# Performance work log

Hardware: AMD Instinct MI355X
Metric: run time of the kernel (lower is better)

The kernel has to match this reference:

```python
import jax, jax.numpy as jnp
import numpy as np

B, L, C, N, DEPTH, OUT = 32, 4096, 128, 64, 4, 1
EPS = 1e-5


def setup_inputs() -> dict:
    key = jax.random.key(0)
    ks = jax.random.split(key, 8)
    x = jax.random.normal(ks[0], (B, L, C), dtype=jnp.float32)
    # S4D parameters, stacked over depth
    # dt log-uniform in [1e-3, 1e-1]
    u = jax.random.uniform(ks[1], (DEPTH, C), dtype=jnp.float32)
    log_dt = u * (np.log(1e-1) - np.log(1e-3)) + np.log(1e-3)
    A_real = jnp.log(0.5 * jnp.ones((DEPTH, C, N), dtype=jnp.float32))  # A = -exp(A_real)+i*A_imag
    A_imag = jnp.broadcast_to(np.pi * jnp.arange(N, dtype=jnp.float32), (DEPTH, C, N)).copy()
    C_re = jax.random.normal(ks[2], (DEPTH, C, N), dtype=jnp.float32) * 0.5
    C_im = jax.random.normal(ks[3], (DEPTH, C, N), dtype=jnp.float32) * 0.5
    Dskip = jax.random.normal(ks[4], (DEPTH, C), dtype=jnp.float32)
    norm_w = jnp.ones((DEPTH, C), dtype=jnp.float32)
    norm_b = jnp.zeros((DEPTH, C), dtype=jnp.float32)
    head_w = jax.random.normal(ks[5], (C, OUT), dtype=jnp.float32) / np.sqrt(C)
    head_b = jnp.zeros((OUT,), dtype=jnp.float32)
    return {"x": x, "log_dt": log_dt, "A_real": A_real, "A_imag": A_imag,
            "C_re": C_re, "C_im": C_im, "Dskip": Dskip,
            "norm_w": norm_w, "norm_b": norm_b, "head_w": head_w, "head_b": head_b}


def _s4d(x, log_dt, A_real, A_imag, C_re, C_im, Dskip):
    # x: [B, L, C]; per-channel diagonal SSM (S4D, ZOH discretization)
    Lx = x.shape[1]
    dt = jnp.exp(log_dt)                               # [C]
    A = -jnp.exp(A_real) + 1j * A_imag                 # [C, N]
    dtA = A * dt[:, None]                              # [C, N]
    Cbar = (C_re + 1j * C_im) * (jnp.exp(dtA) - 1.0) / A  # [C, N] = C * B_bar
    t = jnp.arange(Lx, dtype=jnp.float32)
    # Vandermonde kernel: K[c, l] = 2*Re sum_n Cbar[c,n] * exp(dtA[c,n]*l)
    K = 2.0 * jnp.real(jnp.einsum('cn,cnl->cl', Cbar, jnp.exp(dtA[:, :, None] * t)))  # [C, L]
    # FFT long convolution (causal, linear conv via zero-pad to 2L)
    nfft = 2 * Lx
    xf = jnp.fft.rfft(x, n=nfft, axis=1)               # [B, F, C]
    Kf = jnp.fft.rfft(K, n=nfft, axis=-1)              # [C, F]
    y = jnp.fft.irfft(xf * Kf.T[None], n=nfft, axis=1)[:, :Lx, :]
    return y + x * Dskip                               # D skip connection


def _layernorm(x, w, b):
    mu = jnp.mean(x, axis=-1, keepdims=True)
    var = jnp.mean(jnp.square(x - mu), axis=-1, keepdims=True)
    return (x - mu) * jax.lax.rsqrt(var + EPS) * w + b


def reference(x, log_dt, A_real, A_imag, C_re, C_im, Dskip, norm_w, norm_b, head_w, head_b):
    for d in range(DEPTH):
        residual = x
        y = _s4d(x, log_dt[d], A_real[d], A_imag[d], C_re[d], C_im[d], Dskip[d])
        x = _layernorm(y + residual, norm_w[d], norm_b[d])
    return x @ head_w + head_b                          # [B, L, OUT]
```

## Files before the change

kernel.cpp:

```cpp
#include <hip/hip_runtime.h>
#include <hip/hip_bf16.h>


#define BB     32
#define LL     4096
#define CC     128
#define NN     64
#define DEPTH_ 4
#define EPSV   1e-5f

typedef __attribute__((ext_vector_type(8))) short short8;
typedef __attribute__((ext_vector_type(4))) short short4v;
typedef __attribute__((ext_vector_type(4))) float f32x4;
typedef __hip_bfloat16 bf16;

#define MFMA(a, b, c) __builtin_amdgcn_mfma_f32_16x16x32_bf16(a, b, c, 0, 0, 0)

__device__ __forceinline__ bf16 tobf(float x) { return __float2bfloat16(x); }
__device__ __forceinline__ short bfbits(float x) {
    union { bf16 b; short s; } u; u.b = __float2bfloat16(x); return u.s;
}

__global__ __launch_bounds__(64) void p0_kernel(
    const float* __restrict__ log_dt, const float* __restrict__ A_real,
    const float* __restrict__ A_imag, const float* __restrict__ C_re,
    const float* __restrict__ C_im, float2* __restrict__ lam,
    float2* __restrict__ dta, float2* __restrict__ cb2,
    float2* __restrict__ lamT)
{
    int d = blockIdx.y, c = blockIdx.x, n = threadIdx.x;
    int idx = (d * CC + c) * NN + n;
    float dt  = expf(log_dt[d * CC + c]);
    float Ar  = -expf(A_real[idx]);
    float Ai  = A_imag[idx];
    float dtr = dt * Ar, dti = dt * Ai;
    float e   = expf(dtr);
    float lr  = e * cosf(dti), li = e * sinf(dti);
    float m    = Ar * Ar + Ai * Ai;
    float inv  = 1.0f / m;
    float numr = lr - 1.0f, numi = li;
    float br   = (numr * Ar + numi * Ai) * inv;
    float bi   = (numi * Ar - numr * Ai) * inv;
    float cre  = C_re[idx], cim = C_im[idx];
    lam[idx]  = make_float2(lr, li);
    dta[idx]  = make_float2(dtr, dti);
    cb2[idx]  = make_float2(2.0f * (cre * br - cim * bi),
                            2.0f * (cre * bi + cim * br));
    float eT = expf(64.0f * dtr);
    lamT[idx] = make_float2(eT * cosf(64.0f * dti), eT * sinf(64.0f * dti));
}

__global__ __launch_bounds__(64) void p1_kernel(
    const float2* __restrict__ cb2, const float2* __restrict__ lam,
    float* __restrict__ Kloc)
{
    __shared__ float st[64 * 65];
    int d = blockIdx.y, c = blockIdx.x, n = threadIdx.x;
    float2 p = cb2[(d * CC + c) * NN + n];
    float2 l = lam[(d * CC + c) * NN + n];
    for (int t = 0; t < 64; ++t) {
        st[t * 65 + n] = p.x;
        float nr = p.x * l.x - p.y * l.y;
        p.y = p.x * l.y + p.y * l.x;
        p.x = nr;
    }
    __syncthreads();
    float s = 0.0f;
#pragma unroll 16
    for (int j = 0; j < 64; ++j) s += st[n * 65 + j];
    Kloc[(d * CC + c) * 64 + n] = s;
}

__global__ __launch_bounds__(256) void p2v_kernel(
    const float2* __restrict__ dta, bf16* __restrict__ Vp)
{
    int t = blockIdx.x * 256 + threadIdx.x;
    int e = t & 7, l = (t >> 3) & 63, ks = (t >> 9) & 1;
    int nf = (t >> 10) & 7, c = (t >> 13) & 127, d = t >> 20;
    int q = nf * 16 + (l & 15);
    int k = ks * 32 + (l >> 4) * 8 + e;
    int n = q >> 1;
    float2 a = dta[(d * CC + c) * NN + n];
    float p  = (float)(63 - k);
    float mag = expf(p * a.x);
    float ang = p * a.y;
    float val = (q & 1) ? mag * sinf(ang) : mag * cosf(ang);
    Vp[t] = tobf(val);
}

__global__ __launch_bounds__(256) void p2w_kernel(
    const float2* __restrict__ dta, const float2* __restrict__ cb2,
    const float* __restrict__ Kloc, const float* __restrict__ Dskip,
    bf16* __restrict__ W2p)
{
    int t = blockIdx.x * 256 + threadIdx.x;
    int e = t & 7, l = (t >> 3) & 63;
    int r = t >> 9;
    int ks = r % 6; r /= 6;
    int nf = r & 3; r >>= 2;
    int c  = r & 127;
    int d  = r >> 7;
    int i = nf * 16 + (l & 15);
    int k = ks * 32 + (l >> 4) * 8 + e;
    float val;
    if (k < 64) {
        val = (k <= i) ? Kloc[(d * CC + c) * 64 + (i - k)] : 0.0f;
        if (k == i) val += Dskip[d * CC + c] + 1.0f;
    } else {
        int q = k - 64, n = q >> 1;
        float2 a  = dta[(d * CC + c) * NN + n];
        float2 cb = cb2[(d * CC + c) * NN + n];
        float p   = (float)(i + 1);
        float mag = expf(p * a.x);
        float ang = p * a.y;
        float re = mag * cosf(ang), im = mag * sinf(ang);
        float wre = cb.x * re - cb.y * im;
        float wim = cb.x * im + cb.y * re;
        val = (q & 1) ? -wim : wre;
    }
    W2p[t] = tobf(val);
}

__global__ __launch_bounds__(256) void transpose_kernel(
    const float* __restrict__ x, bf16* __restrict__ xt)
{
    __shared__ float t[64][65];
    int ct = blockIdx.x, lt = blockIdx.y, b = blockIdx.z;
    int tx = threadIdx.x & 63, ty = threadIdx.x >> 6;
    const size_t xbase = ((size_t)b * LL + (size_t)lt * 64) * CC + (size_t)ct * 64;
#pragma unroll
    for (int i = 0; i < 16; ++i)
        t[ty + 4 * i][tx] = x[xbase + (size_t)(ty + 4 * i) * CC + tx];
    __syncthreads();
    const size_t obase = ((size_t)b * CC + (size_t)ct * 64) * LL + (size_t)lt * 64;
#pragma unroll
    for (int i = 0; i < 16; ++i)
        xt[obase + (size_t)(ty + 4 * i) * LL + tx] = tobf(t[tx][ty + 4 * i]);
}

__global__ __launch_bounds__(512) void ks_kernel(
    const bf16* __restrict__ u, bf16* __restrict__ v,
    const bf16* __restrict__ Vp, const bf16* __restrict__ W2p,
    const float2* __restrict__ lamT)
{
    const int c  = blockIdx.x;
    const int w  = threadIdx.x >> 6;
    const int l  = threadIdx.x & 63;
    const int b  = blockIdx.y * 8 + w;
    const int bc = b * CC + c;
    const bf16* xrow = u + (size_t)bc * LL;
    bf16*       vrow = v + (size_t)bc * LL;

    __shared__ short Wl[8192 + 12288];
    __shared__ short Sp[8][16 * 136];

    {
        uint4*       dst  = (uint4*)Wl;
        const uint4* srcV = (const uint4*)(Vp  + (size_t)c * 8192);
        const uint4* srcW = (const uint4*)(W2p + (size_t)c * 12288);
        int tid = threadIdx.x;
#pragma unroll
        for (int i = 0; i < 2; ++i)
            dst[tid + 512 * i] = srcV[tid + 512 * i];
#pragma unroll
        for (int i = 0; i < 3; ++i)
            dst[1024 + tid + 512 * i] = srcW[tid + 512 * i];
    }
    __syncthreads();

    short* S = Sp[w];
    const short* W2l = Wl + 8192;
    const int mloc = l & 15;
    const int koff = (l >> 4) * 8;
    float2 lt = lamT[c * NN + l];
    float sr = 0.f, si = 0.f;

#pragma unroll 1
    for (int g = 0; g < 4; ++g) {
        const bf16* xg = xrow + (g * 16 + mloc) * 64;

        {
            short8 xf0 = *(const short8*)(xg + koff);
            short8 xf1 = *(const short8*)(xg + 32 + koff);
#pragma unroll
            for (int h = 0; h < 2; ++h) {
                f32x4 acc[4];
#pragma unroll
                for (int j = 0; j < 4; ++j) acc[j] = (f32x4){0.f, 0.f, 0.f, 0.f};
#pragma unroll
                for (int j = 0; j < 4; ++j) {
                    int nf = h * 4 + j;
                    short8 vf0 = *(const short8*)(&Wl[((nf * 2 + 0) * 64 + l) * 8]);
                    short8 vf1 = *(const short8*)(&Wl[((nf * 2 + 1) * 64 + l) * 8]);
                    acc[j] = MFMA(vf0, xf0, acc[j]);
                    acc[j] = MFMA(vf1, xf1, acc[j]);
                }
#pragma unroll
                for (int j = 0; j < 4; ++j) {
                    int nf = h * 4 + j;
                    short4v t;
                    t[0] = bfbits(acc[j][0]); t[1] = bfbits(acc[j][1]);
                    t[2] = bfbits(acc[j][2]); t[3] = bfbits(acc[j][3]);
                    *(short4v*)(&S[mloc * 136 + nf * 16 + (l >> 4) * 4]) = t;
                }
            }
        }
        asm volatile("" ::: "memory");

#pragma unroll
        for (int k = 0; k < 16; ++k) {
            uint pk = *(const uint*)(&S[k * 136 + 2 * l]);
            union { short2 s2; uint uu; } o;
            o.s2.x = bfbits(sr); o.s2.y = bfbits(si);
            *(uint*)(&S[k * 136 + 2 * l]) = o.uu;
            float pr = __uint_as_float(pk << 16);
            float pi = __uint_as_float(pk & 0xffff0000u);
            float nr = fmaf(lt.x, sr, fmaf(-lt.y, si, pr));
            si = fmaf(lt.x, si, fmaf(lt.y, sr, pi));
            sr = nr;
        }
        asm volatile("" ::: "memory");

        f32x4 o[4];
#pragma unroll
        for (int nf = 0; nf < 4; ++nf) o[nf] = (f32x4){0.f, 0.f, 0.f, 0.f};
#pragma unroll
        for (int ks = 0; ks < 6; ++ks) {
            short8 xf;
            if (ks < 2)
                xf = *(const short8*)(xg + ks * 32 + koff);
            else
                xf = *(const short8*)(&S[mloc * 136 + (ks - 2) * 32 + koff]);
#pragma unroll
            for (int nf = 0; nf < 4; ++nf) {
                short8 wf = *(const short8*)(&W2l[((nf * 6 + ks) * 64 + l) * 8]);
                o[nf] = MFMA(wf, xf, o[nf]);
            }
        }
#pragma unroll
        for (int nf = 0; nf < 4; ++nf) {
            short4v t;
            t[0] = bfbits(o[nf][0]); t[1] = bfbits(o[nf][1]);
            t[2] = bfbits(o[nf][2]); t[3] = bfbits(o[nf][3]);
            *(short4v*)(vrow + (g * 16 + mloc) * 64 + nf * 16 + (l >> 4) * 4) = t;
        }
    }
}

__global__ __launch_bounds__(256) void ln_kernel(
    const bf16* __restrict__ v, bf16* __restrict__ outx,
    const float* __restrict__ w, const float* __restrict__ bta,
    const float* __restrict__ headw, const float* __restrict__ headb,
    float* __restrict__ fout, int isfinal)
{
    __shared__ float tile[CC][65];
    __shared__ float r1[4][64];
    __shared__ float r2[4][64];
    __shared__ float mrs[2][64];
    int b    = blockIdx.y;
    int l0   = blockIdx.x * 64;
    int lane = threadIdx.x & 63;
    int cg   = threadIdx.x >> 6;
    float sum = 0.0f, sq = 0.0f;
#pragma unroll
    for (int ci = 0; ci < 32; ++ci) {
        int c = cg * 32 + ci;
        float val = __bfloat162float(v[((size_t)b * CC + c) * LL + l0 + lane]);
        tile[c][lane] = val;
        sum += val;
        sq = fmaf(val, val, sq);
    }
    r1[cg][lane] = sum;
    r2[cg][lane] = sq;
    __syncthreads();
    if (cg == 0) {
        float s = r1[0][lane] + r1[1][lane] + r1[2][lane] + r1[3][lane];
        float q = r2[0][lane] + r2[1][lane] + r2[2][lane] + r2[3][lane];
        float mean = s * (1.0f / CC);
        float var  = q * (1.0f / CC) - mean * mean;
        mrs[0][lane] = mean;
        mrs[1][lane] = rsqrtf(var + EPSV);
    }
    __syncthreads();
    float mean = mrs[0][lane], rstd = mrs[1][lane];
    if (!isfinal) {
#pragma unroll
        for (int ci = 0; ci < 32; ++ci) {
            int c = cg * 32 + ci;
            float o = (tile[c][lane] - mean) * rstd * w[c] + bta[c];
            outx[((size_t)b * CC + c) * LL + l0 + lane] = tobf(o);
        }
    } else {
        float h = 0.0f;
#pragma unroll
        for (int ci = 0; ci < 32; ++ci) {
            int c = cg * 32 + ci;
            float o = (tile[c][lane] - mean) * rstd * w[c] + bta[c];
            h = fmaf(o, headw[c], h);
        }
        __syncthreads();
        r1[cg][lane] = h;
        __syncthreads();
        if (cg == 0)
            fout[(size_t)b * LL + l0 + lane] =
                r1[0][lane] + r1[1][lane] + r1[2][lane] + r1[3][lane] + headb[0];
    }
}

extern "C" void kernel_launch(void* const* d_in, const int* in_sizes, int n_in,
                              void* d_out, int out_size, void* d_ws, size_t ws_size,
                              hipStream_t stream)
{
    const float* x      = (const float*)d_in[0];
    const float* log_dt = (const float*)d_in[1];
    const float* A_real = (const float*)d_in[2];
    const float* A_imag = (const float*)d_in[3];
    const float* C_re   = (const float*)d_in[4];
    const float* C_im   = (const float*)d_in[5];
    const float* Dskip  = (const float*)d_in[6];
    const float* norm_w = (const float*)d_in[7];
    const float* norm_b = (const float*)d_in[8];
    const float* head_w = (const float*)d_in[9];
    const float* head_b = (const float*)d_in[10];
    float* out = (float*)d_out;

    const size_t DCN = (size_t)DEPTH_ * CC * NN;
    const size_t BCL = (size_t)BB * CC * LL;

    float2* lam  = (float2*)d_ws;
    float2* dta  = lam + DCN;
    float2* cb2  = dta + DCN;
    float2* lamT = cb2 + DCN;
    float*  Kloc = (float*)(lamT + DCN);
    bf16*   u    = (bf16*)(Kloc + (size_t)DEPTH_ * CC * 64);
    bf16*   v    = u + BCL;
    bf16*   Vp   = v + BCL;
    bf16*   W2p  = Vp + (size_t)DEPTH_ * CC * 8192;

    p0_kernel<<<dim3(CC, DEPTH_), 64, 0, stream>>>(
        log_dt, A_real, A_imag, C_re, C_im, lam, dta, cb2, lamT);
    p1_kernel<<<dim3(CC, DEPTH_), 64, 0, stream>>>(cb2, lam, Kloc);
    p2v_kernel<<<(DEPTH_ * CC * 8192) / 256, 256, 0, stream>>>(dta, Vp);
    p2w_kernel<<<(DEPTH_ * CC * 12288) / 256, 256, 0, stream>>>(
        dta, cb2, Kloc, Dskip, W2p);
    transpose_kernel<<<dim3(CC / 64, LL / 64, BB), 256, 0, stream>>>(x, u);

    for (int d = 0; d < DEPTH_; ++d) {
        ks_kernel<<<dim3(CC, BB / 8), 512, 0, stream>>>(
            u, v, Vp + (size_t)d * CC * 8192, W2p + (size_t)d * CC * 12288,
            lamT + (size_t)d * CC * NN);
        ln_kernel<<<dim3(LL / 64, BB), 256, 0, stream>>>(
            v, u, norm_w + d * CC, norm_b + d * CC,
            head_w, head_b, out, (d == DEPTH_ - 1) ? 1 : 0);
    }
}
```

Before: 185.9 us.

## Fuse LayerNorm apply into next S4 layer via precomputed row stats

Intermediate LayerNorms are no longer written out as a full normalized tensor. A light stats kernel now computes only the per-position mean and rstd, and the next ks_kernel applies the normalization to its input fragments on load. Intermediate layers therefore skip one full read-modify-write pass of the B×C×L activation. Activation buffers ping-pong between layers, and the x fragments are kept in registers instead of being reloaded for the second MFMA stage. The trade-off is an extra small stats buffer, plus stats loads and FMA work inside the ks inner loop.

```diff
diff --git a/kernel.cpp b/kernel.cpp
--- a/kernel.cpp
+++ b/kernel.cpp
@@ -19,6 +19,9 @@
 __device__ __forceinline__ bf16 tobf(float x) { return __float2bfloat16(x); }
 __device__ __forceinline__ short bfbits(float x) {
     union { bf16 b; short s; } u; u.b = __float2bfloat16(x); return u.s;
+}
+__device__ __forceinline__ float frombits(short s) {
+    return __uint_as_float(((uint)(ushort)s) << 16);
 }
 
 __global__ __launch_bounds__(64) void p0_kernel(
@@ -138,10 +141,53 @@
         xt[obase + (size_t)(ty + 4 * i) * LL + tx] = tobf(t[tx][ty + 4 * i]);
 }
 
+__global__ __launch_bounds__(256) void stats_kernel(
+    const bf16* __restrict__ v, float2* __restrict__ st)
+{
+    __shared__ float rs[4][256];
+    __shared__ float rq[4][256];
+    int b  = blockIdx.y;
+    int l0 = blockIdx.x * 256;
+    int lt = threadIdx.x & 63;
+    int cg = threadIdx.x >> 6;
+    const short* vv = (const short*)v;
+    float s[4] = {0.f, 0.f, 0.f, 0.f};
+    float q[4] = {0.f, 0.f, 0.f, 0.f};
+#pragma unroll
+    for (int ci = 0; ci < 32; ++ci) {
+        int c = cg * 32 + ci;
+        short4v r = *(const short4v*)(&vv[((size_t)b * CC + c) * LL + l0 + lt * 4]);
+#pragma unroll
+        for (int j = 0; j < 4; ++j) {
+            float f = frombits(r[j]);
+            s[j] += f;
+            q[j] = fmaf(f, f, q[j]);
+        }
+    }
+#pragma unroll
+    for (int j = 0; j < 4; ++j) {
+        rs[cg][lt * 4 + j] = s[j];
+        rq[cg][lt * 4 + j] = q[j];
+    }
+    __syncthreads();
+    if (cg == 0) {
+#pragma unroll
+        for (int j = 0; j < 4; ++j) {
+            int li = lt * 4 + j;
+            float ts = rs[0][li] + rs[1][li] + rs[2][li] + rs[3][li];
+            float tq = rq[0][li] + rq[1][li] + rq[2][li] + rq[3][li];
+            float mean = ts * (1.0f / CC);
+            float var  = tq * (1.0f / CC) - mean * mean;
+            st[(size_t)b * LL + l0 + li] = make_float2(mean, rsqrtf(var + EPSV));
+        }
+    }
+}
+
 __global__ __launch_bounds__(512) void ks_kernel(
     const bf16* __restrict__ u, bf16* __restrict__ v,
     const bf16* __restrict__ Vp, const bf16* __restrict__ W2p,
-    const float2* __restrict__ lamT)
+    const float2* __restrict__ lamT, const float2* __restrict__ st,
+    const float* __restrict__ nw, const float* __restrict__ nb)
 {
     const int c  = blockIdx.x;
     const int w  = threadIdx.x >> 6;
@@ -175,34 +221,48 @@
     float2 lt = lamT[c * NN + l];
     float sr = 0.f, si = 0.f;
 
+    const float2* stb = st ? (st + (size_t)b * LL) : nullptr;
+    float wc = 0.f, bcf = 0.f;
+    if (st) { wc = nw[c]; bcf = nb[c]; }
+
 #pragma unroll 1
     for (int g = 0; g < 4; ++g) {
-        const bf16* xg = xrow + (g * 16 + mloc) * 64;
-
-        {
-            short8 xf0 = *(const short8*)(xg + koff);
-            short8 xf1 = *(const short8*)(xg + 32 + koff);
-#pragma unroll
-            for (int h = 0; h < 2; ++h) {
-                f32x4 acc[4];
-#pragma unroll
-                for (int j = 0; j < 4; ++j) acc[j] = (f32x4){0.f, 0.f, 0.f, 0.f};
-#pragma unroll
-                for (int j = 0; j < 4; ++j) {
-                    int nf = h * 4 + j;
-                    short8 vf0 = *(const short8*)(&Wl[((nf * 2 + 0) * 64 + l) * 8]);
-                    short8 vf1 = *(const short8*)(&Wl[((nf * 2 + 1) * 64 + l) * 8]);
-                    acc[j] = MFMA(vf0, xf0, acc[j]);
-                    acc[j] = MFMA(vf1, xf1, acc[j]);
-                }
-#pragma unroll
-                for (int j = 0; j < 4; ++j) {
-                    int nf = h * 4 + j;
-                    short4v t;
-                    t[0] = bfbits(acc[j][0]); t[1] = bfbits(acc[j][1]);
-                    t[2] = bfbits(acc[j][2]); t[3] = bfbits(acc[j][3]);
-                    *(short4v*)(&S[mloc * 136 + nf * 16 + (l >> 4) * 4]) = t;
-                }
+        const int lbase = (g * 16 + mloc) * 64 + koff;
+        const bf16* xg = xrow + lbase;
+
+        short8 xf0 = *(const short8*)(xg);
+        short8 xf1 = *(const short8*)(xg + 32);
+        if (stb) {
+#pragma unroll
+            for (int e = 0; e < 8; ++e) {
+                float2 s0 = stb[lbase + e];
+                float2 s1 = stb[lbase + 32 + e];
+                float a0 = s0.y * wc, a1 = s1.y * wc;
+                xf0[e] = bfbits(fmaf(frombits(xf0[e]), a0, fmaf(-s0.x, a0, bcf)));
+                xf1[e] = bfbits(fmaf(frombits(xf1[e]), a1, fmaf(-s1.x, a1, bcf)));
+            }
+        }
+
+#pragma unroll
+        for (int h = 0; h < 2; ++h) {
+            f32x4 acc[4];
+#pragma unroll
+            for (int j = 0; j < 4; ++j) acc[j] = (f32x4){0.f, 0.f, 0.f, 0.f};
+#pragma unroll
+            for (int j = 0; j < 4; ++j) {
+                int nf = h * 4 + j;
+                short8 vf0 = *(const short8*)(&Wl[((nf * 2 + 0) * 64 + l) * 8]);
+                short8 vf1 = *(const short8*)(&Wl[((nf * 2 + 1) * 64 + l) * 8]);
+                acc[j] = MFMA(vf0, xf0, acc[j]);
+                acc[j] = MFMA(vf1, xf1, acc[j]);
+            }
+#pragma unroll
+            for (int j = 0; j < 4; ++j) {
+                int nf = h * 4 + j;
+                short4v t;
+                t[0] = bfbits(acc[j][0]); t[1] = bfbits(acc[j][1]);
+                t[2] = bfbits(acc[j][2]); t[3] = bfbits(acc[j][3]);
+                *(short4v*)(&S[mloc * 136 + nf * 16 + (l >> 4) * 4]) = t;
             }
         }
         asm volatile("" ::: "memory");
@@ -227,10 +287,9 @@
 #pragma unroll
         for (int ks = 0; ks < 6; ++ks) {
             short8 xf;
-            if (ks < 2)
-                xf = *(const short8*)(xg + ks * 32 + koff);
-            else
-                xf = *(const short8*)(&S[mloc * 136 + (ks - 2) * 32 + koff]);
+            if (ks == 0)      xf = xf0;
+            else if (ks == 1) xf = xf1;
+            else              xf = *(const short8*)(&S[mloc * 136 + (ks - 2) * 32 + koff]);
 #pragma unroll
             for (int nf = 0; nf < 4; ++nf) {
                 short8 wf = *(const short8*)(&W2l[((nf * 6 + ks) * 64 + l) * 8]);
@@ -248,10 +307,10 @@
 }
 
 __global__ __launch_bounds__(256) void ln_kernel(
-    const bf16* __restrict__ v, bf16* __restrict__ outx,
+    const bf16* __restrict__ v,
     const float* __restrict__ w, const float* __restrict__ bta,
     const float* __restrict__ headw, const float* __restrict__ headb,
-    float* __restrict__ fout, int isfinal)
+    float* __restrict__ fout)
 {
     __shared__ float tile[CC][65];
     __shared__ float r1[4][64];
@@ -283,28 +342,19 @@
     }
     __syncthreads();
     float mean = mrs[0][lane], rstd = mrs[1][lane];
-    if (!isfinal) {
-#pragma unroll
-        for (int ci = 0; ci < 32; ++ci) {
-            int c = cg * 32 + ci;
-            float o = (tile[c][lane] - mean) * rstd * w[c] + bta[c];
-            outx[((size_t)b * CC + c) * LL + l0 + lane] = tobf(o);
-        }
-    } else {
-        float h = 0.0f;
-#pragma unroll
-        for (int ci = 0; ci < 32; ++ci) {
-            int c = cg * 32 + ci;
-            float o = (tile[c][lane] - mean) * rstd * w[c] + bta[c];
-            h = fmaf(o, headw[c], h);
-        }
-        __syncthreads();
-        r1[cg][lane] = h;
-        __syncthreads();
-        if (cg == 0)
-            fout[(size_t)b * LL + l0 + lane] =
-                r1[0][lane] + r1[1][lane] + r1[2][lane] + r1[3][lane] + headb[0];
-    }
+    float h = 0.0f;
+#pragma unroll
+    for (int ci = 0; ci < 32; ++ci) {
+        int c = cg * 32 + ci;
+        float o = (tile[c][lane] - mean) * rstd * w[c] + bta[c];
+        h = fmaf(o, headw[c], h);
+    }
+    __syncthreads();
+    r1[cg][lane] = h;
+    __syncthreads();
+    if (cg == 0)
+        fout[(size_t)b * LL + l0 + lane] =
+            r1[0][lane] + r1[1][lane] + r1[2][lane] + r1[3][lane] + headb[0];
 }
 
 extern "C" void kernel_launch(void* const* d_in, const int* in_sizes, int n_in,
@@ -332,10 +382,11 @@
     float2* cb2  = dta + DCN;
     float2* lamT = cb2 + DCN;
     float*  Kloc = (float*)(lamT + DCN);
-    bf16*   u    = (bf16*)(Kloc + (size_t)DEPTH_ * CC * 64);
-    bf16*   v    = u + BCL;
-    bf16*   Vp   = v + BCL;
+    bf16*   A    = (bf16*)(Kloc + (size_t)DEPTH_ * CC * 64);
+    bf16*   Bb   = A + BCL;
+    bf16*   Vp   = Bb + BCL;
     bf16*   W2p  = Vp + (size_t)DEPTH_ * CC * 8192;
+    float2* stbuf = (float2*)(W2p + (size_t)DEPTH_ * CC * 12288);
 
     p0_kernel<<<dim3(CC, DEPTH_), 64, 0, stream>>>(
         log_dt, A_real, A_imag, C_re, C_im, lam, dta, cb2, lamT);
@@ -343,14 +394,21 @@
     p2v_kernel<<<(DEPTH_ * CC * 8192) / 256, 256, 0, stream>>>(dta, Vp);
     p2w_kernel<<<(DEPTH_ * CC * 12288) / 256, 256, 0, stream>>>(
         dta, cb2, Kloc, Dskip, W2p);
-    transpose_kernel<<<dim3(CC / 64, LL / 64, BB), 256, 0, stream>>>(x, u);
-
-    for (int d = 0; d < DEPTH_; ++d) {
+    transpose_kernel<<<dim3(CC / 64, LL / 64, BB), 256, 0, stream>>>(x, A);
+
+    ks_kernel<<<dim3(CC, BB / 8), 512, 0, stream>>>(
+        A, Bb, Vp, W2p, lamT, nullptr, nullptr, nullptr);
+    bf16* src = Bb;
+    bf16* dst = A;
+    for (int d = 1; d < DEPTH_; ++d) {
+        stats_kernel<<<dim3(LL / 256, BB), 256, 0, stream>>>(src, stbuf);
         ks_kernel<<<dim3(CC, BB / 8), 512, 0, stream>>>(
-            u, v, Vp + (size_t)d * CC * 8192, W2p + (size_t)d * CC * 12288,
-            lamT + (size_t)d * CC * NN);
-        ln_kernel<<<dim3(LL / 64, BB), 256, 0, stream>>>(
-            v, u, norm_w + d * CC, norm_b + d * CC,
-            head_w, head_b, out, (d == DEPTH_ - 1) ? 1 : 0);
-    }
-}
+            src, dst, Vp + (size_t)d * CC * 8192, W2p + (size_t)d * CC * 12288,
+            lamT + (size_t)d * CC * NN, stbuf,
+            norm_w + (d - 1) * CC, norm_b + (d - 1) * CC);
+        bf16* tmp = src; src = dst; dst = tmp;
+    }
+    ln_kernel<<<dim3(LL / 64, BB), 256, 0, stream>>>(
+        src, norm_w + (DEPTH_ - 1) * CC, norm_b + (DEPTH_ - 1) * CC,
+        head_w, head_b, out);
+}
```

Result: no change. 184.5 us (-0.7%).
